# Optimization experiments

Measured on AMD Instinct MI355X. Metric: run time of the kernel, lower is better.

The kernel has to match this reference:

```python
import jax, jax.numpy as jnp
import numpy as np

BUCKET_SIZE = 512
# Classic perfect-spatial-hashing primes (PSH / Teschner et al.)
P1 = np.uint32(73856093)
P2 = np.uint32(19349663)
P3 = np.uint32(83492791)
P4 = np.uint32(2654435761)  # mixes batch id into the hash


def setup_inputs() -> dict:
    key = jax.random.key(0)
    k1, k2 = jax.random.split(key)
    N, B = 4_000_000, 16
    coords = jax.random.normal(k1, (N, 3), dtype=jnp.float32) * 10.0
    seps = jnp.sort(jax.random.randint(k2, (B,), 0, N, dtype=jnp.int32))
    return {"coords": coords, "seps": seps, "hash_op": 1}


def reference(coords, seps, hash_op):
    """Hash-based bucket scatter with padding (PSHScatterLayer forward).

    Each point is voxelized, spatially hashed (mixed with its batch id from
    `seps`) into one of num_buckets buckets; points are written into a padded
    [pad_to, 3] buffer at slot = bucket * BUCKET_SIZE + within-bucket rank.
    Points overflowing a bucket are dropped (finite-capacity bucket counter).
    Deterministic rank (arrival order) replaces the CUDA atomic counter.
    """
    N = coords.shape[0]
    pad_to = ((N + BUCKET_SIZE - 1) // BUCKET_SIZE) * BUCKET_SIZE
    num_buckets = pad_to // BUCKET_SIZE

    # voxelize + spatial hash (non-differentiable index path)
    vox = jnp.floor(jax.lax.stop_gradient(coords)).astype(jnp.int32).astype(jnp.uint32)  # [N,3]
    batch_id = jnp.searchsorted(seps, jnp.arange(N, dtype=seps.dtype), side='right').astype(jnp.uint32)
    h = (vox[:, 0] * P1) ^ (vox[:, 1] * P2) ^ (vox[:, 2] * P3) ^ (batch_id * P4)
    h = h + jnp.uint32(hash_op)
    bucket = (h % jnp.uint32(num_buckets)).astype(jnp.int32)  # [N]

    # per-bucket counts and within-bucket rank (stable order = arrival order)
    counts = jax.ops.segment_sum(jnp.ones((N,), jnp.int32), bucket, num_segments=num_buckets)
    starts = jnp.cumsum(counts) - counts                      # [num_buckets]
    order = jnp.argsort(bucket)                               # stable in jax
    rank_sorted = jnp.arange(N, dtype=jnp.int32) - starts[bucket[order]]
    rank = jnp.zeros((N,), jnp.int32).at[order].set(rank_sorted)

    slot = bucket * BUCKET_SIZE + rank
    idx = jnp.where(rank < BUCKET_SIZE, slot, pad_to)         # out-of-range -> dropped
    scattered_coord = jnp.zeros((pad_to, 3), coords.dtype).at[idx].set(coords, mode='drop')
    return scattered_coord, counts, bucket
```

## Files before the change

kernel.cpp:

```cpp
#include <hip/hip_runtime.h>
#include <stdint.h>

#define PR1 73856093u
#define PR2 19349663u
#define PR3 83492791u
#define PR4 2654435761u
#define GS  32
#define PPT 4
#define BBITS 13

__device__ __forceinline__ uint32_t fastmod(uint32_t h, uint32_t d, double inv) {
    uint32_t q = (uint32_t)((double)h * inv);
    int32_t r = (int32_t)(h - q * d);
    if (r >= (int32_t)d) r -= d;
    if (r < 0) r += d;
    return (uint32_t)r;
}

__device__ __forceinline__ int chunk_of(int bi, int C) {
    return ((C & 7) == 0) ? ((bi & 7) * (C >> 3) + (bi >> 3)) : bi;
}

__global__ void k_bucket_hist(const float* __restrict__ coords,
                              const int* __restrict__ seps, int B,
                              const int* __restrict__ hash_op_p,
                              int N, int NB, int C, int chunk, double invNB,
                              float* __restrict__ out_bucket,
                              uint16_t* __restrict__ ch) {
    extern __shared__ int hist[];
    __shared__ int s_seps[1024];
    const int tid = threadIdx.x;
    for (int i = tid; i < NB; i += blockDim.x) hist[i] = 0;
    const int Bc = B < 1024 ? B : 1024;
    for (int j = tid; j < Bc; j += blockDim.x) s_seps[j] = seps[j];
    __syncthreads();

    const uint32_t hop = (uint32_t)hash_op_p[0];
    const int c = chunk_of(blockIdx.x, C);
    const int start = c * chunk;
    const int end   = min(start + chunk, N);
    int bid = 0;
    for (int i = start + tid; i < end; i += blockDim.x) {
        while (bid < B) {
            const int sv = (bid < 1024) ? s_seps[bid] : seps[bid];
            if (sv <= i) bid++; else break;
        }
        const float x = coords[3 * (size_t)i + 0];
        const float y = coords[3 * (size_t)i + 1];
        const float z = coords[3 * (size_t)i + 2];
        const uint32_t vx = (uint32_t)(int32_t)floorf(x);
        const uint32_t vy = (uint32_t)(int32_t)floorf(y);
        const uint32_t vz = (uint32_t)(int32_t)floorf(z);
        uint32_t h = vx * PR1 ^ vy * PR2 ^ vz * PR3 ^ ((uint32_t)bid * PR4);
        h += hop;
        const uint32_t b = fastmod(h, (uint32_t)NB, invNB);
        out_bucket[i] = (float)b;
        atomicAdd(&hist[(int)b], 1);
    }
    __syncthreads();
    uint16_t* dst = ch + (size_t)c * NB;
    for (int i = tid; i < NB; i += blockDim.x) dst[i] = (uint16_t)hist[i];
}

__global__ void k_scan_group(uint16_t* __restrict__ ch, int* __restrict__ Sg,
                             int C, int NB) {
    const int b = blockIdx.x * blockDim.x + threadIdx.x;
    if (b >= NB) return;
    const int g  = blockIdx.y;
    const int c0 = g * GS;
    const int c1 = min(c0 + GS, C);
    int run = 0;
    for (int c = c0; c < c1; c++) {
        const size_t idx = (size_t)c * NB + b;
        const int v = ch[idx];
        ch[idx] = (uint16_t)(run < 512 ? run : 512);
        run += v;
    }
    Sg[(size_t)g * NB + b] = run;
}

__global__ void k_scan_tops(int* __restrict__ Sg, int G, int NB,
                            float* __restrict__ out_counts,
                            float* __restrict__ out_sc) {
    const int b = blockIdx.x * blockDim.x + threadIdx.x;
    if (b >= NB) return;
    int run = 0;
    for (int g = 0; g < G; g++) {
        const size_t idx = (size_t)g * NB + b;
        const int v = Sg[idx];
        Sg[idx] = run;
        run += v;
    }
    out_counts[b] = (float)run;
    const int c0 = run < 512 ? run : 512;
    float* p = out_sc + ((size_t)b * 512 + c0) * 3;
    for (int j = c0; j < 512; j++) {
        p[0] = 0.f; p[1] = 0.f; p[2] = 0.f;
        p += 3;
    }
}

__global__ __launch_bounds__(256, 4)
void k_scatter(const float* __restrict__ coords,
               const float* __restrict__ bucket_f,
               const uint16_t* __restrict__ ch,
               const int* __restrict__ Sg,
               int N, int NB, int C, int chunk,
               float* __restrict__ out_sc) {
    extern __shared__ int hist[];
    const int tid = threadIdx.x;
    const int c = chunk_of(blockIdx.x, C);
    const int g = c / GS;
    const uint16_t* r1 = ch + (size_t)c * NB;
    const int*      r2 = Sg + (size_t)g * NB;
    for (int i = tid; i < NB; i += blockDim.x) hist[i] = (int)r1[i] + r2[i];
    __syncthreads();

    const int start = c * chunk;
    const int end   = min(start + chunk, N);
    const int len   = end > start ? end - start : 0;
    const int per_round = (int)blockDim.x * PPT;
    const int rounds = (len + per_round - 1) / per_round;
    const int lane = tid & 63;
    const int wv   = tid >> 6;
    const int nw   = (int)blockDim.x >> 6;
    const unsigned long long ltmask = ((unsigned long long)1 << lane) - 1;

    for (int rd = 0; rd < rounds; rd++) {
        const int wbase = start + rd * per_round + wv * (64 * PPT);
        int bs[PPT], leader[PPT], cntv[PPT], rnk[PPT];
        float cx[PPT], cy[PPT], cz[PPT];

        #pragma unroll
        for (int s = 0; s < PPT; s++) {
            const int i = wbase + s * 64 + lane;
            const bool v = (i < end);
            bs[s] = v ? (int)bucket_f[i] : NB;
            cx[s] = v ? coords[3 * (size_t)i + 0] : 0.f;
            cy[s] = v ? coords[3 * (size_t)i + 1] : 0.f;
            cz[s] = v ? coords[3 * (size_t)i + 2] : 0.f;
        }

        #pragma unroll
        for (int s = 0; s < PPT; s++) {
            const int b = bs[s];
            unsigned long long mm = ~0ull;
            #pragma unroll
            for (int k = 0; k < BBITS; k++) {
                const unsigned long long blt = __ballot(((b >> k) & 1) != 0);
                mm &= ((b >> k) & 1) ? blt : ~blt;
            }
            leader[s] = (int)__builtin_ctzll(mm);
            cntv[s]   = (int)__builtin_popcountll(mm);
            rnk[s]    = (int)__builtin_popcountll(mm & ltmask);
        }

        int basev[PPT];
        for (int w = 0; w < nw; w++) {
            if (wv == w) {
                #pragma unroll
                for (int s = 0; s < PPT; s++) {
                    int old = 0;
                    if (bs[s] < NB && lane == leader[s])
                        old = atomicAdd(&hist[bs[s]], cntv[s]);
                    basev[s] = __shfl(old, leader[s], 64);
                }
            }
            __syncthreads();
        }

        #pragma unroll
        for (int s = 0; s < PPT; s++) {
            if (bs[s] < NB) {
                const int r = basev[s] + rnk[s];
                if (r < 512) {
                    float* p = out_sc + ((size_t)bs[s] * 512 + r) * 3;
                    p[0] = cx[s]; p[1] = cy[s]; p[2] = cz[s];
                }
            }
        }
    }
}

extern "C" void kernel_launch(void* const* d_in, const int* in_sizes, int n_in,
                              void* d_out, int out_size, void* d_ws, size_t ws_size,
                              hipStream_t stream) {
    const float* coords  = (const float*)d_in[0];
    const int*   seps    = (const int*)d_in[1];
    const int*   hash_op = (const int*)d_in[2];

    const int N = in_sizes[0] / 3;
    const int B = in_sizes[1];
    const int pad_to = ((N + 511) / 512) * 512;
    const int NB = pad_to / 512;

    float* out        = (float*)d_out;
    float* out_counts = out + (size_t)pad_to * 3;
    float* out_bucket = out_counts + NB;

    int C = 1024;
    while (C > 8) {
        const int G_ = (C + GS - 1) / GS;
        if ((size_t)C * NB * 2 + (size_t)G_ * NB * 4 <= ws_size) break;
        C -= 8;
    }
    const int G = (C + GS - 1) / GS;
    const int chunk = (N + C - 1) / C;
    uint16_t* ch = (uint16_t*)d_ws;
    int* Sg = (int*)((char*)d_ws + (((size_t)C * NB * 2 + 15) & ~(size_t)15));
    const size_t lds = (size_t)NB * sizeof(int);
    const double invNB = 1.0 / (double)NB;

    k_bucket_hist<<<C, 256, lds, stream>>>(coords, seps, B, hash_op, N, NB, C,
                                           chunk, invNB, out_bucket, ch);
    dim3 g2a((NB + 255) / 256, G);
    k_scan_group<<<g2a, 256, 0, stream>>>(ch, Sg, C, NB);
    k_scan_tops<<<(NB + 255) / 256, 256, 0, stream>>>(Sg, G, NB, out_counts, out);
    k_scatter<<<C, 256, lds, stream>>>(coords, out_bucket, ch, Sg,
                                       N, NB, C, chunk, out);
}
```

Measured before the change: 217.7 us.

## Vectorize histogram loads and replace scatter barrier loop with wave turn ticket

In the histogram kernel each thread now handles four consecutive points, reading coords as three float4 and writing the bucket ids as one float4, so memory access is wider. In the scatter kernel the per-wave serialized loop of __syncthreads is replaced by an LDS turn counter. Each wave spins until its turn, does its atomics, then passes the turn to the next wave, so waves no longer stall at block-wide barriers. The chunk size is rounded to a multiple of four for alignment. The spin-wait relies on waves making forward progress and on LDS ordering, which risks deadlock or ordering bugs, and rounding the chunk changes how work is split across blocks.

```diff
diff --git a/kernel.cpp b/kernel.cpp
--- a/kernel.cpp
+++ b/kernel.cpp
@@ -21,12 +21,13 @@
     return ((C & 7) == 0) ? ((bi & 7) * (C >> 3) + (bi >> 3)) : bi;
 }
 
-__global__ void k_bucket_hist(const float* __restrict__ coords,
-                              const int* __restrict__ seps, int B,
-                              const int* __restrict__ hash_op_p,
-                              int N, int NB, int C, int chunk, double invNB,
-                              float* __restrict__ out_bucket,
-                              uint16_t* __restrict__ ch) {
+__global__ __launch_bounds__(256)
+void k_bucket_hist(const float* __restrict__ coords,
+                   const int* __restrict__ seps, int B,
+                   const int* __restrict__ hash_op_p,
+                   int N, int NB, int C, int chunk, double invNB,
+                   float* __restrict__ out_bucket,
+                   uint16_t* __restrict__ ch) {
     extern __shared__ int hist[];
     __shared__ int s_seps[1024];
     const int tid = threadIdx.x;
@@ -40,22 +41,51 @@
     const int start = c * chunk;
     const int end   = min(start + chunk, N);
     int bid = 0;
-    for (int i = start + tid; i < end; i += blockDim.x) {
-        while (bid < B) {
-            const int sv = (bid < 1024) ? s_seps[bid] : seps[bid];
-            if (sv <= i) bid++; else break;
-        }
-        const float x = coords[3 * (size_t)i + 0];
-        const float y = coords[3 * (size_t)i + 1];
-        const float z = coords[3 * (size_t)i + 2];
-        const uint32_t vx = (uint32_t)(int32_t)floorf(x);
-        const uint32_t vy = (uint32_t)(int32_t)floorf(y);
-        const uint32_t vz = (uint32_t)(int32_t)floorf(z);
-        uint32_t h = vx * PR1 ^ vy * PR2 ^ vz * PR3 ^ ((uint32_t)bid * PR4);
-        h += hop;
-        const uint32_t b = fastmod(h, (uint32_t)NB, invNB);
-        out_bucket[i] = (float)b;
-        atomicAdd(&hist[(int)b], 1);
+    for (int i0 = start + tid * 4; i0 < end; i0 += (int)blockDim.x * 4) {
+        const int navail = end - i0;
+        float xs[4], ys[4], zs[4];
+        if (navail >= 4) {
+            const float4* cp = (const float4*)(coords + 3 * (size_t)i0);
+            const float4 a = cp[0], b4 = cp[1], c4 = cp[2];
+            xs[0] = a.x;  ys[0] = a.y;  zs[0] = a.z;
+            xs[1] = a.w;  ys[1] = b4.x; zs[1] = b4.y;
+            xs[2] = b4.z; ys[2] = b4.w; zs[2] = c4.x;
+            xs[3] = c4.y; ys[3] = c4.z; zs[3] = c4.w;
+        } else {
+            #pragma unroll
+            for (int p = 0; p < 4; p++) {
+                const int i = i0 + p;
+                if (i < end) {
+                    xs[p] = coords[3 * (size_t)i + 0];
+                    ys[p] = coords[3 * (size_t)i + 1];
+                    zs[p] = coords[3 * (size_t)i + 2];
+                } else { xs[p] = ys[p] = zs[p] = 0.f; }
+            }
+        }
+        float bf[4];
+        #pragma unroll
+        for (int p = 0; p < 4; p++) {
+            const int i = i0 + p;
+            if (i < end) {
+                while (bid < B) {
+                    const int sv = (bid < 1024) ? s_seps[bid] : seps[bid];
+                    if (sv <= i) bid++; else break;
+                }
+                const uint32_t vx = (uint32_t)(int32_t)floorf(xs[p]);
+                const uint32_t vy = (uint32_t)(int32_t)floorf(ys[p]);
+                const uint32_t vz = (uint32_t)(int32_t)floorf(zs[p]);
+                uint32_t h = vx * PR1 ^ vy * PR2 ^ vz * PR3 ^ ((uint32_t)bid * PR4);
+                h += hop;
+                const uint32_t b = fastmod(h, (uint32_t)NB, invNB);
+                bf[p] = (float)b;
+                atomicAdd(&hist[(int)b], 1);
+            } else bf[p] = 0.f;
+        }
+        if (navail >= 4) {
+            *(float4*)(out_bucket + i0) = make_float4(bf[0], bf[1], bf[2], bf[3]);
+        } else {
+            for (int p = 0; p < navail; p++) out_bucket[i0 + p] = bf[p];
+        }
     }
     __syncthreads();
     uint16_t* dst = ch + (size_t)c * NB;
@@ -108,12 +138,14 @@
                int N, int NB, int C, int chunk,
                float* __restrict__ out_sc) {
     extern __shared__ int hist[];
+    volatile int* vturn = hist + NB;
     const int tid = threadIdx.x;
     const int c = chunk_of(blockIdx.x, C);
     const int g = c / GS;
     const uint16_t* r1 = ch + (size_t)c * NB;
     const int*      r2 = Sg + (size_t)g * NB;
     for (int i = tid; i < NB; i += blockDim.x) hist[i] = (int)r1[i] + r2[i];
+    if (tid == 0) hist[NB] = 0;
     __syncthreads();
 
     const int start = c * chunk;
@@ -155,19 +187,24 @@
             rnk[s]    = (int)__builtin_popcountll(mm & ltmask);
         }
 
+        const int target = rd * nw + wv;
+        while (*vturn < target) __builtin_amdgcn_s_sleep(1);
+        __builtin_amdgcn_sched_barrier(0);
+
+        int oldv[PPT];
+        #pragma unroll
+        for (int s = 0; s < PPT; s++) {
+            oldv[s] = 0;
+            if (bs[s] < NB && lane == leader[s])
+                oldv[s] = atomicAdd(&hist[bs[s]], cntv[s]);
+        }
+        asm volatile("s_waitcnt lgkmcnt(0)" ::: "memory");
+        if (lane == 0) *vturn = target + 1;
+
         int basev[PPT];
-        for (int w = 0; w < nw; w++) {
-            if (wv == w) {
-                #pragma unroll
-                for (int s = 0; s < PPT; s++) {
-                    int old = 0;
-                    if (bs[s] < NB && lane == leader[s])
-                        old = atomicAdd(&hist[bs[s]], cntv[s]);
-                    basev[s] = __shfl(old, leader[s], 64);
-                }
-            }
-            __syncthreads();
-        }
+        #pragma unroll
+        for (int s = 0; s < PPT; s++)
+            basev[s] = __shfl(oldv[s], leader[s], 64);
 
         #pragma unroll
         for (int s = 0; s < PPT; s++) {
@@ -205,10 +242,11 @@
         C -= 8;
     }
     const int G = (C + GS - 1) / GS;
-    const int chunk = (N + C - 1) / C;
+    int chunk = (N + C - 1) / C;
+    chunk = (chunk + 3) & ~3;
     uint16_t* ch = (uint16_t*)d_ws;
     int* Sg = (int*)((char*)d_ws + (((size_t)C * NB * 2 + 15) & ~(size_t)15));
-    const size_t lds = (size_t)NB * sizeof(int);
+    const size_t lds = ((size_t)NB + 1) * sizeof(int);
     const double invNB = 1.0 / (double)NB;
 
     k_bucket_hist<<<C, 256, lds, stream>>>(coords, seps, B, hash_op, N, NB, C,
```

After: 208.8 us. -4.1%, faster.
